# Optimization experiments

Hardware: AMD Instinct MI355X
Metric: run time of the kernel (lower is better)

Reference implementation:

```python
import jax, jax.numpy as jnp
import numpy as np

DIM = 256
DQK = DIM // 8
LN_SHAPE = (256, 4, 32, 32)


def setup_inputs() -> dict:
    key = jax.random.key(0)
    ks = jax.random.split(key, 12)
    B, C, Z, H, W = 4, 256, 4, 32, 32
    s = 0.02
    return {
        "x": jax.random.normal(ks[0], (B, C, Z, H, W), jnp.float32),
        "y": jax.random.normal(ks[1], (B, C, Z, H, W), jnp.float32),
        "Wq": jax.random.normal(ks[2], (DQK, C), jnp.float32) * s,
        "bq": jnp.zeros((DQK,), jnp.float32),
        "Wk": jax.random.normal(ks[3], (DQK, C), jnp.float32) * s,
        "bk": jnp.zeros((DQK,), jnp.float32),
        "Wv": jax.random.normal(ks[4], (C, C), jnp.float32) * s,
        "bv": jnp.zeros((C,), jnp.float32),
        "W1": jax.random.normal(ks[5], (C, C), jnp.float32) * s,
        "b1": jnp.zeros((C,), jnp.float32),
        "W2": jax.random.normal(ks[6], (C, C), jnp.float32) * s,
        "b2": jnp.zeros((C,), jnp.float32),
        "gamma": jnp.ones(LN_SHAPE, jnp.float32),
        "beta": jnp.zeros(LN_SHAPE, jnp.float32),
    }


def reference(x, y, Wq, bq, Wk, bk, Wv, bv, W1, b1, W2, b2, gamma, beta):
    B, C, Z, H, W = x.shape
    N = Z * H * W
    scale = (C // 8) ** (-0.5)

    def proj(t, Wm, bm):  # 1x1x1 conv3d == channel linear: [B,C,N] -> [B,out,N]
        return jnp.einsum('oc,bcn->bon', Wm, t.reshape(B, C, N)) + bm[None, :, None]

    def branch(a, b):
        q = proj(a, Wq, bq).transpose(0, 2, 1) * scale  # [B,N,dqk]
        k = proj(b, Wk, bk)                             # [B,dqk,N]
        v = proj(b, Wv, bv)                             # [B,C,N]
        attn = jax.nn.softmax(jnp.einsum('bnd,bdm->bnm', q, k), axis=-1)  # [B,N,N]
        out = jnp.einsum('bcm,bnm->bcn', v, attn).reshape(B, C, Z, H, W)
        h = out.transpose(0, 2, 3, 4, 1)  # [B,Z,H,W,C]
        h = jnp.maximum(jnp.einsum('bzhwc,oc->bzhwo', h, W1) + b1, 0.0)
        h = jnp.einsum('bzhwc,oc->bzhwo', h, W2) + b2
        h = h.transpose(0, 4, 1, 2, 3)  # [B,C,Z,H,W]
        mu = h.mean(axis=(1, 2, 3, 4), keepdims=True)
        var = h.var(axis=(1, 2, 3, 4), keepdims=True)
        return (h - mu) / jnp.sqrt(var + 1e-5) * gamma + beta

    return branch(x, y), branch(y, x)
```

## Files before the change

### kernel.cpp

```cpp
#include <hip/hip_runtime.h>

#define C_DIM 256
#define N_TOK 4096
#define DQK_  32
#define SCALE_Q 0.17677669529663687f

typedef unsigned short u16;
typedef __attribute__((ext_vector_type(8))) short bf16x8;
typedef __attribute__((ext_vector_type(16))) float f32x16;

__device__ __forceinline__ u16 f2b(float f) {
  unsigned u = __builtin_bit_cast(unsigned, f);
  unsigned r = (u + 0x7fffu + ((u >> 16) & 1u)) >> 16;
  return (u16)r;
}
__device__ __forceinline__ unsigned splitw(float v) {
  unsigned h = f2b(v);
  float hf = __builtin_bit_cast(float, h << 16);
  unsigned l = f2b(v - hf);
  return h | (l << 16);
}
__device__ __forceinline__ unsigned cvtpk(float lo, float hi) {
  unsigned r;
  asm("v_cvt_pk_bf16_f32 %0, %1, %2" : "=v"(r) : "v"(lo), "v"(hi));
  return r;
}

__global__ __launch_bounds__(256) void prep_kernel(
    const float* __restrict__ x, const float* __restrict__ y,
    u16* __restrict__ xhi, u16* __restrict__ yhi,
    const float* __restrict__ Wv, const float* __restrict__ W1, const float* __restrict__ W2,
    const float* __restrict__ Wq, const float* __restrict__ Wk,
    u16* __restrict__ Wvh, u16* __restrict__ Wvl,
    u16* __restrict__ W1h, u16* __restrict__ W1l,
    u16* __restrict__ W2h, u16* __restrict__ W2l,
    u16* __restrict__ Wqh, u16* __restrict__ Wql,
    u16* __restrict__ Wkh, u16* __restrict__ Wkl)
{
  __shared__ float tile[64][65];
  int bid = blockIdx.x;
  int t = threadIdx.x;
  if (bid < 2048) {
    int bx = bid & 63, by = (bid >> 6) & 3, z = bid >> 8;
    const float* src = (z < 4 ? x : y) + (size_t)(z & 3) * C_DIM * N_TOK;
    u16* dhi = (z < 4 ? xhi : yhi) + (size_t)(z & 3) * N_TOK * C_DIM;
    int m0 = bx * 64, c0 = by * 64;
    #pragma unroll
    for (int pp = 0; pp < 4; ++pp) {
      int c = pp*16 + (t >> 4), m = (t & 15)*4;
      float4 v = *(const float4*)(src + (size_t)(c0 + c)*N_TOK + m0 + m);
      tile[c][m] = v.x; tile[c][m+1] = v.y; tile[c][m+2] = v.z; tile[c][m+3] = v.w;
    }
    __syncthreads();
    int m = t >> 2, cg = (t & 3) * 16;
    unsigned hw[8];
    #pragma unroll
    for (int j2 = 0; j2 < 8; ++j2)
      hw[j2] = (unsigned)f2b(tile[cg + 2*j2][m]) | ((unsigned)f2b(tile[cg + 2*j2 + 1][m]) << 16);
    size_t base = (size_t)(m0 + m)*C_DIM + c0 + cg;
    *(uint4*)(dhi + base)     = make_uint4(hw[0], hw[1], hw[2], hw[3]);
    *(uint4*)(dhi + base + 8) = make_uint4(hw[4], hw[5], hw[6], hw[7]);
  } else {
    int wb = bid - 2048;
    int which, base;
    if (wb < 768) { which = wb >> 8; base = wb & 255; }
    else if (wb < 800) { which = 3; base = wb - 768; }
    else { which = 4; base = wb - 800; }
    const float* src = which == 0 ? Wv : which == 1 ? W1 : which == 2 ? W2 : which == 3 ? Wq : Wk;
    u16* dhi = which == 0 ? Wvh : which == 1 ? W1h : which == 2 ? W2h : which == 3 ? Wqh : Wkh;
    u16* dlo = which == 0 ? Wvl : which == 1 ? W1l : which == 2 ? W2l : which == 3 ? Wql : Wkl;
    int idx = base*256 + t;
    unsigned s = splitw(src[idx]);
    dhi[idx] = (u16)(s & 0xffffu);
    dlo[idx] = (u16)(s >> 16);
  }
}

__device__ __forceinline__ void gemm_v_body(
    char* lds, int bx, int by, int bb,
    const u16* __restrict__ Ahi0, const u16* __restrict__ Ahi1, size_t aStride,
    const u16* __restrict__ Bhi, const u16* __restrict__ Blo,
    const float* __restrict__ bias, u16* __restrict__ OutBase, size_t oStride)
{
  const u16* Ah = (bb < 4 ? Ahi0 : Ahi1) + (size_t)(bb & 3) * aStride;
  int l0 = bx * 128;
  int s0 = by * 128;
  u16* Ob = OutBase + (size_t)bb * oStride;

  char* ldsAh = lds;
  char* ldsBh = lds + 16384;
  char* ldsBl = lds + 32768;

  int t = threadIdx.x;
  int w = t >> 6, lane = t & 63, g = lane >> 5, l31 = lane & 31;
  int lw = (w & 1) * 64, sw = (w >> 1) * 64;
  int swz = (l31 & 7) << 4;

  f32x16 acc[2][2];
  #pragma unroll
  for (int i = 0; i < 2; ++i)
    #pragma unroll
    for (int j = 0; j < 2; ++j)
      #pragma unroll
      for (int r = 0; r < 16; ++r) acc[i][j][r] = 0.f;

  uint4 rAh[4], rBh[4], rBl[4];
  #pragma unroll
  for (int c = 0; c < 4; ++c) {
    int idx = c*256 + t, row = idx >> 3, slot = idx & 7;
    rAh[c] = *(const uint4*)(Ah  + (size_t)(l0 + row)*C_DIM + slot*8);
    rBh[c] = *(const uint4*)(Bhi + (size_t)(s0 + row)*C_DIM + slot*8);
    rBl[c] = *(const uint4*)(Blo + (size_t)(s0 + row)*C_DIM + slot*8);
  }
  for (int bk = 0; bk < 4; ++bk) {
    __syncthreads();
    #pragma unroll
    for (int c = 0; c < 4; ++c) {
      int idx = c*256 + t, row = idx >> 3, slot = idx & 7;
      int off = row*128 + ((slot*16) ^ ((row & 7) << 4));
      *(uint4*)(ldsAh + off) = rAh[c];
      *(uint4*)(ldsBh + off) = rBh[c];
      *(uint4*)(ldsBl + off) = rBl[c];
    }
    __syncthreads();
    if (bk < 3) {
      #pragma unroll
      for (int c = 0; c < 4; ++c) {
        int idx = c*256 + t, row = idx >> 3, slot = idx & 7;
        rAh[c] = *(const uint4*)(Ah  + (size_t)(l0 + row)*C_DIM + (bk+1)*64 + slot*8);
        rBh[c] = *(const uint4*)(Bhi + (size_t)(s0 + row)*C_DIM + (bk+1)*64 + slot*8);
        rBl[c] = *(const uint4*)(Blo + (size_t)(s0 + row)*C_DIM + (bk+1)*64 + slot*8);
      }
    }
    #pragma unroll
    for (int ks = 0; ks < 4; ++ks) {
      int ko = ks*32 + g*16;
      bf16x8 ah0 = *(const bf16x8*)(ldsAh + (lw + l31)*128      + (ko ^ swz));
      bf16x8 ah1 = *(const bf16x8*)(ldsAh + (lw + 32 + l31)*128 + (ko ^ swz));
      bf16x8 bh0 = *(const bf16x8*)(ldsBh + (sw + l31)*128      + (ko ^ swz));
      bf16x8 bh1 = *(const bf16x8*)(ldsBh + (sw + 32 + l31)*128 + (ko ^ swz));
      bf16x8 bl0 = *(const bf16x8*)(ldsBl + (sw + l31)*128      + (ko ^ swz));
      bf16x8 bl1 = *(const bf16x8*)(ldsBl + (sw + 32 + l31)*128 + (ko ^ swz));
      acc[0][0] = __builtin_amdgcn_mfma_f32_32x32x16_bf16(ah0, bh0, acc[0][0], 0,0,0);
      acc[0][1] = __builtin_amdgcn_mfma_f32_32x32x16_bf16(ah0, bh1, acc[0][1], 0,0,0);
      acc[1][0] = __builtin_amdgcn_mfma_f32_32x32x16_bf16(ah1, bh0, acc[1][0], 0,0,0);
      acc[1][1] = __builtin_amdgcn_mfma_f32_32x32x16_bf16(ah1, bh1, acc[1][1], 0,0,0);
      acc[0][0] = __builtin_amdgcn_mfma_f32_32x32x16_bf16(ah0, bl0, acc[0][0], 0,0,0);
      acc[0][1] = __builtin_amdgcn_mfma_f32_32x32x16_bf16(ah0, bl1, acc[0][1], 0,0,0);
      acc[1][0] = __builtin_amdgcn_mfma_f32_32x32x16_bf16(ah1, bl0, acc[1][0], 0,0,0);
      acc[1][1] = __builtin_amdgcn_mfma_f32_32x32x16_bf16(ah1, bl1, acc[1][1], 0,0,0);
    }
  }

  for (int h = 0; h < 2; ++h) {
    __syncthreads();
    if ((w >> 1) == h) {
      #pragma unroll
      for (int j = 0; j < 2; ++j) {
        int sl = j*32 + l31;
        float bv = bias[s0 + h*64 + sl];
        #pragma unroll
        for (int i = 0; i < 2; ++i)
          #pragma unroll
          for (int q = 0; q < 4; ++q) {
            int lbase = lw + i*32 + 8*q + 4*g;
            unsigned w0 = (unsigned)f2b(acc[i][j][q*4+0] + bv)
                        | ((unsigned)f2b(acc[i][j][q*4+1] + bv) << 16);
            unsigned w1 = (unsigned)f2b(acc[i][j][q*4+2] + bv)
                        | ((unsigned)f2b(acc[i][j][q*4+3] + bv) << 16);
            *(uint2*)(lds + sl*272 + lbase*2) = make_uint2(w0, w1);
          }
      }
    }
    __syncthreads();
    #pragma unroll
    for (int p = 0; p < 4; ++p) {
      int s = p*16 + (t >> 4), col = (t & 15)*8;
      uint4 v = *(const uint4*)(lds + s*272 + col*2);
      *(uint4*)(Ob + (size_t)(s0 + h*64 + s)*(size_t)N_TOK + l0 + col) = v;
    }
  }
}

__device__ __forceinline__ void proj_qk_body(
    char* lds, int bx, int which, int bb,
    const u16* __restrict__ xs_hi, const u16* __restrict__ ys_hi,
    const u16* __restrict__ Wqh, const u16* __restrict__ Wql,
    const u16* __restrict__ Wkh, const u16* __restrict__ Wkl,
    const float* __restrict__ bq, const float* __restrict__ bk,
    u16* __restrict__ Qout, u16* __restrict__ Kout)
{
  int branch = bb >> 2, batch = bb & 3;
  int n0 = bx * 256;
  const u16* Asrc = (which == 0 ? (branch ? ys_hi : xs_hi) : (branch ? xs_hi : ys_hi))
                    + (size_t)batch * N_TOK * C_DIM;
  const u16* Bh = which ? Wkh : Wqh;
  const u16* Bl = which ? Wkl : Wql;
  const float* bias = which ? bk : bq;
  float sc = which ? 1.0f : SCALE_Q;
  u16* out = (which ? Kout : Qout) + (size_t)bb * N_TOK * DQK_;

  char* ldsA  = lds;
  char* ldsBh = lds + 32768;
  char* ldsBl = lds + 40960;

  int t = threadIdx.x, w = t >> 6, lane = t & 63, g = lane >> 5, l31 = lane & 31;
  int swz = (l31 & 7) << 4;

  f32x16 acc[2];
  #pragma unroll
  for (int i = 0; i < 2; ++i)
    #pragma unroll
    for (int r = 0; r < 16; ++r) acc[i][r] = 0.f;

  uint4 rA[8]; uint4 rBh, rBl;
  #pragma unroll
  for (int c = 0; c < 8; ++c) {
    int idx = c*256 + t, row = idx >> 3, slot = idx & 7;
    rA[c] = *(const uint4*)(Asrc + (size_t)(n0 + row)*C_DIM + slot*8);
  }
  { int row = t >> 3, slot = t & 7;
    rBh = *(const uint4*)(Bh + (size_t)row*C_DIM + slot*8);
    rBl = *(const uint4*)(Bl + (size_t)row*C_DIM + slot*8); }

  for (int bk = 0; bk < 4; ++bk) {
    __syncthreads();
    #pragma unroll
    for (int c = 0; c < 8; ++c) {
      int idx = c*256 + t, row = idx >> 3, slot = idx & 7;
      *(uint4*)(ldsA + row*128 + ((slot*16) ^ ((row & 7) << 4))) = rA[c];
    }
    { int row = t >> 3, slot = t & 7;
      int off = row*128 + ((slot*16) ^ ((row & 7) << 4));
      *(uint4*)(ldsBh + off) = rBh;
      *(uint4*)(ldsBl + off) = rBl; }
    __syncthreads();
    if (bk < 3) {
      #pragma unroll
      for (int c = 0; c < 8; ++c) {
        int idx = c*256 + t, row = idx >> 3, slot = idx & 7;
        rA[c] = *(const uint4*)(Asrc + (size_t)(n0 + row)*C_DIM + (bk+1)*64 + slot*8);
      }
      { int row = t >> 3, slot = t & 7;
        rBh = *(const uint4*)(Bh + (size_t)row*C_DIM + (bk+1)*64 + slot*8);
        rBl = *(const uint4*)(Bl + (size_t)row*C_DIM + (bk+1)*64 + slot*8); }
    }
    #pragma unroll
    for (int ks = 0; ks < 4; ++ks) {
      int ko = ks*32 + g*16;
      bf16x8 a0 = *(const bf16x8*)(ldsA + (w*64 + l31)*128      + (ko ^ swz));
      bf16x8 a1 = *(const bf16x8*)(ldsA + (w*64 + 32 + l31)*128 + (ko ^ swz));
      bf16x8 bh = *(const bf16x8*)(ldsBh + l31*128 + (ko ^ swz));
      bf16x8 bl = *(const bf16x8*)(ldsBl + l31*128 + (ko ^ swz));
      acc[0] = __builtin_amdgcn_mfma_f32_32x32x16_bf16(a0, bh, acc[0], 0,0,0);
      acc[1] = __builtin_amdgcn_mfma_f32_32x32x16_bf16(a1, bh, acc[1], 0,0,0);
      acc[0] = __builtin_amdgcn_mfma_f32_32x32x16_bf16(a0, bl, acc[0], 0,0,0);
      acc[1] = __builtin_amdgcn_mfma_f32_32x32x16_bf16(a1, bl, acc[1], 0,0,0);
    }
  }
  float bv = bias[l31];
  #pragma unroll
  for (int sub = 0; sub < 2; ++sub)
    #pragma unroll
    for (int r = 0; r < 16; ++r) {
      int n = w*64 + sub*32 + (r&3) + 8*(r>>2) + 4*g;
      out[(size_t)(n0 + n)*DQK_ + l31] = f2b((acc[sub][r] + bv) * sc);
    }
}

__global__ __launch_bounds__(256) void pv_qk_kernel(
    const u16* __restrict__ xs_hi, const u16* __restrict__ ys_hi,
    const u16* __restrict__ Wvh, const u16* __restrict__ Wvl,
    const u16* __restrict__ Wqh, const u16* __restrict__ Wql,
    const u16* __restrict__ Wkh, const u16* __restrict__ Wkl,
    const float* __restrict__ bv, const float* __restrict__ bq, const float* __restrict__ bk,
    u16* __restrict__ Vt, u16* __restrict__ Qout, u16* __restrict__ Kout)
{
  __shared__ __align__(16) char lds[49152];
  int bid = blockIdx.x;
  const size_t AS = (size_t)N_TOK * C_DIM;
  if (bid < 512) {
    int bx = bid & 31, by = (bid >> 5) & 1, bb = bid >> 6;
    gemm_v_body(lds, bx, by, bb, ys_hi, xs_hi, AS, Wvh, Wvl, bv, Vt, AS);
  } else {
    int pb = bid - 512;
    int bx = pb & 15, which = (pb >> 4) & 1, bb = pb >> 5;
    proj_qk_body(lds, bx, which, bb, xs_hi, ys_hi, Wqh, Wql, Wkh, Wkl, bq, bk, Qout, Kout);
  }
}

__global__ __launch_bounds__(512) void attn_fused_kernel(
    const u16* __restrict__ Qg, const u16* __restrict__ Kg,
    const u16* __restrict__ Vtg, u16* __restrict__ Ohi)
{
  int id = blockIdx.x;
  int bb = id & 7;
  int n0 = (id >> 3) * 128;
  const u16* Qb = Qg + (size_t)bb * N_TOK * DQK_;
  const u16* Kb = Kg + (size_t)bb * N_TOK * DQK_;
  const u16* Vb = Vtg + (size_t)bb * C_DIM * N_TOK;
  u16* Ohb = Ohi + (size_t)bb * N_TOK * C_DIM;

  __shared__ __align__(16) u16 Kl[2][2][4*64*8];
  __shared__ __align__(16) u16 Vl[2][256*128];

  int t = threadIdx.x;
  int w = t >> 6;
  int grp = w >> 2;
  int wg = w & 3;
  int t4 = t & 255;
  int lane = t & 63, g = lane >> 5, l31 = lane & 31;

  bf16x8 qf0 = *(const bf16x8*)(Qb + (size_t)(n0 + wg*32 + l31)*DQK_ + g*8);
  bf16x8 qf1 = *(const bf16x8*)(Qb + (size_t)(n0 + wg*32 + l31)*DQK_ + 16 + g*8);

  f32x16 acc[8];
  #pragma unroll
  for (int ct = 0; ct < 8; ++ct)
    #pragma unroll
    for (int r = 0; r < 16; ++r) acc[ct][r] = 0.f;

  float L = 0.f;

  bf16x8 stK, stV[8];
  const u16* kSrc = Kb + (size_t)(grp*32*64 + (t4>>7)*32 + (t4&31))*DQK_
                       + ((t4>>6)&1)*16 + ((t4>>5)&1)*8;
  const int vCol0 = grp*32*64;
  stK = *(const bf16x8*)(kSrc);
  #pragma unroll
  for (int i = 0; i < 8; ++i) {
    int q = i*256 + t4;
    stV[i] = *(const bf16x8*)(Vb + (size_t)(q >> 3)*N_TOK + vCol0 + (q & 7)*8);
  }

  u16* VlG = Vl[grp];

  *(bf16x8*)(Kl[grp][0] + t4*8) = stK;
  #pragma unroll
  for (int i = 0; i < 8; ++i) {
    int q = i*256 + t4;
    int c = q >> 3, slot = q & 7;
    *(bf16x8*)((char*)VlG + c*256 + ((slot*16) ^ ((c & 15) << 4))) = stV[i];
  }
  __syncthreads();

  int h = 0;
  for (int mt = 0; mt < 32; ++mt) {
    const u16* KlG = Kl[grp][h];
    f32x16 z;
    #pragma unroll
    for (int r = 0; r < 16; ++r) z[r] = 0.f;
    bf16x8 ka = *(const bf16x8*)(KlG + (0*64 + lane)*8);
    bf16x8 kb = *(const bf16x8*)(KlG + (1*64 + lane)*8);
    bf16x8 kc = *(const bf16x8*)(KlG + (2*64 + lane)*8);
    bf16x8 kd = *(const bf16x8*)(KlG + (3*64 + lane)*8);
    f32x16 st0 = __builtin_amdgcn_mfma_f32_32x32x16_bf16(ka, qf0, z, 0,0,0);
    st0 = __builtin_amdgcn_mfma_f32_32x32x16_bf16(kb, qf1, st0, 0,0,0);
    f32x16 st1 = __builtin_amdgcn_mfma_f32_32x32x16_bf16(kc, qf0, z, 0,0,0);
    st1 = __builtin_amdgcn_mfma_f32_32x32x16_bf16(kd, qf1, st1, 0,0,0);

    if (mt + 1 < 32) {
      stK = *(const bf16x8*)(kSrc + (size_t)(mt+1)*64*DQK_);
      #pragma unroll
      for (int i = 0; i < 8; ++i) {
        int q = i*256 + t4;
        stV[i] = *(const bf16x8*)(Vb + (size_t)(q >> 3)*N_TOK + vCol0 + (mt+1)*64 + (q & 7)*8);
      }
    }

    float ps = 0.f;
    uint4 pav[4];
    #pragma unroll
    for (int msub = 0; msub < 2; ++msub) {
      f32x16 sv = msub ? st1 : st0;
      float p[16];
      #pragma unroll
      for (int r = 0; r < 16; ++r)
        p[r] = __expf(fminf(sv[r], 30.f));
      float q0 = (p[0]+p[1]) + (p[2]+p[3]);
      float q1 = (p[4]+p[5]) + (p[6]+p[7]);
      float q2 = (p[8]+p[9]) + (p[10]+p[11]);
      float q3 = (p[12]+p[13]) + (p[14]+p[15]);
      ps += (q0+q1) + (q2+q3);
      unsigned k0a = cvtpk(p[0],  p[1]),  k0b = cvtpk(p[2],  p[3]);
      unsigned k1a = cvtpk(p[4],  p[5]),  k1b = cvtpk(p[6],  p[7]);
      unsigned k2a = cvtpk(p[8],  p[9]),  k2b = cvtpk(p[10], p[11]);
      unsigned k3a = cvtpk(p[12], p[13]), k3b = cvtpk(p[14], p[15]);
      unsigned X1a = g ? k0a : k1a, X1b = g ? k0b : k1b;
      unsigned X2a = g ? k2a : k3a, X2b = g ? k2b : k3b;
      X1a = __shfl_xor(X1a, 32); X1b = __shfl_xor(X1b, 32);
      X2a = __shfl_xor(X2a, 32); X2b = __shfl_xor(X2b, 32);
      pav[msub*2]     = g ? make_uint4(X1a, X1b, k1a, k1b)
                          : make_uint4(k0a, k0b, X1a, X1b);
      pav[msub*2 + 1] = g ? make_uint4(X2a, X2b, k3a, k3b)
                          : make_uint4(k2a, k2b, X2a, X2b);
    }
    ps += __shfl_xor(ps, 32);
    L += ps;

    __builtin_amdgcn_s_setprio(1);
    #pragma unroll
    for (int ks = 0; ks < 4; ++ks) {
      bf16x8 pa = __builtin_bit_cast(bf16x8, pav[ks]);
      #pragma unroll
      for (int ct = 0; ct < 8; ++ct) {
        bf16x8 vv = *(const bf16x8*)((char*)VlG + (ct*32 + l31)*256
                     + ((h*128 + ks*32 + g*16) ^ ((l31 & 15) << 4)));
        acc[ct] = __builtin_amdgcn_mfma_f32_32x32x16_bf16(pa, vv, acc[ct], 0,0,0);
      }
    }
    __builtin_amdgcn_s_setprio(0);

    if (mt + 1 < 32) {
      *(bf16x8*)(Kl[grp][h ^ 1] + t4*8) = stK;
      #pragma unroll
      for (int i = 0; i < 8; ++i) {
        int q = i*256 + t4;
        int c = q >> 3, slot = q & 7;
        *(bf16x8*)((char*)VlG + c*256 + (((h ^ 1)*128 + slot*16) ^ ((c & 15) << 4))) = stV[i];
      }
    }
    __syncthreads();
    h ^= 1;
  }

  float* mb = (float*)Kl;
  mb[t] = L;
  __syncthreads();
  float Ln = L + mb[t ^ 256];

  float* vb = (float*)Vl;
  #pragma unroll
  for (int pass = 0; pass < 2; ++pass) {
    __syncthreads();
    if (grp == 1) {
      #pragma unroll
      for (int cc = 0; cc < 4; ++cc) {
        int ct = pass*4 + cc;
        #pragma unroll
        for (int r = 0; r < 16; ++r)
          vb[(cc*256 + t4)*16 + r] = acc[ct][r];
      }
    }
    __syncthreads();
    if (grp == 0) {
      #pragma unroll
      for (int cc = 0; cc < 4; ++cc) {
        int ct = pass*4 + cc;
        #pragma unroll
        for (int r = 0; r < 16; ++r)
          acc[ct][r] += vb[(cc*256 + t4)*16 + r];
      }
    }
  }

  if (grp == 0) {
    float lr = 1.0f / Ln;
    float lrr[16];
    #pragma unroll
    for (int r = 0; r < 16; ++r)
      lrr[r] = __shfl(lr, (r&3) + 8*(r>>2) + 4*g, 32);
    #pragma unroll
    for (int ct = 0; ct < 8; ++ct) {
      #pragma unroll
      for (int r = 0; r < 16; ++r) {
        int nr = (r&3) + 8*(r>>2) + 4*g;
        size_t off = (size_t)(n0 + wg*32 + nr)*C_DIM + ct*32 + l31;
        Ohb[off] = f2b(acc[ct][r] * lrr[r]);
      }
    }
  }
}

__global__ __launch_bounds__(512) void ffn_fused_kernel(
    const u16* __restrict__ Ohi, const u16* __restrict__ W1h, const u16* __restrict__ W1l,
    const u16* __restrict__ W2h, const u16* __restrict__ W2l,
    const float* __restrict__ b1, const float* __restrict__ b2,
    float* __restrict__ out, float* __restrict__ part)
{
  int bb = blockIdx.y;
  int l0 = blockIdx.x * 128;
  const u16* Ah = Ohi + (size_t)bb * N_TOK * C_DIM;
  float* Ob = out + (size_t)bb * (size_t)N_TOK * C_DIM;

  __shared__ __align__(16) char lds[147456];
  char* ldsH1 = lds;
  char* ldsA  = lds + 65536;
  char* ldsBh = lds + 81920;
  char* ldsBl = lds + 114688;

  int t = threadIdx.x;
  int w = t >> 6, lane = t & 63, g = lane >> 5, l31 = lane & 31;
  int lw = (w & 1) * 64, sw = (w >> 1) * 64;
  int swz = (l31 & 7) << 4;

  f32x16 acc[2][2];
  #pragma unroll
  for (int i = 0; i < 2; ++i)
    #pragma unroll
    for (int j = 0; j < 2; ++j)
      #pragma unroll
      for (int r = 0; r < 16; ++r) acc[i][j][r] = 0.f;

  uint4 rA[2], rBh[4], rBl[4];
  #pragma unroll
  for (int c = 0; c < 2; ++c) {
    int u = c*512 + t, row = u >> 3, slot = u & 7;
    rA[c] = *(const uint4*)(Ah + (size_t)(l0 + row)*C_DIM + slot*8);
  }
  #pragma unroll
  for (int c = 0; c < 4; ++c) {
    int u = c*512 + t, row = u >> 3, slot = u & 7;
    rBh[c] = *(const uint4*)(W1h + (size_t)row*C_DIM + slot*8);
    rBl[c] = *(const uint4*)(W1l + (size_t)row*C_DIM + slot*8);
  }
  for (int bk = 0; bk < 4; ++bk) {
    __syncthreads();
    #pragma unroll
    for (int c = 0; c < 2; ++c) {
      int u = c*512 + t, row = u >> 3, slot = u & 7;
      *(uint4*)(ldsA + row*128 + ((slot*16) ^ ((row & 7) << 4))) = rA[c];
    }
    #pragma unroll
    for (int c = 0; c < 4; ++c) {
      int u = c*512 + t, row = u >> 3, slot = u & 7;
      int off = row*128 + ((slot*16) ^ ((row & 7) << 4));
      *(uint4*)(ldsBh + off) = rBh[c];
      *(uint4*)(ldsBl + off) = rBl[c];
    }
    __syncthreads();
    if (bk < 3) {
      #pragma unroll
      for (int c = 0; c < 2; ++c) {
        int u = c*512 + t, row = u >> 3, slot = u & 7;
        rA[c] = *(const uint4*)(Ah + (size_t)(l0 + row)*C_DIM + (bk+1)*64 + slot*8);
      }
      #pragma unroll
      for (int c = 0; c < 4; ++c) {
        int u = c*512 + t, row = u >> 3, slot = u & 7;
        rBh[c] = *(const uint4*)(W1h + (size_t)row*C_DIM + (bk+1)*64 + slot*8);
        rBl[c] = *(const uint4*)(W1l + (size_t)row*C_DIM + (bk+1)*64 + slot*8);
      }
    }
    #pragma unroll
    for (int ks = 0; ks < 4; ++ks) {
      int ko = ks*32 + g*16;
      bf16x8 ah0 = *(const bf16x8*)(ldsA + (lw + l31)*128      + (ko ^ swz));
      bf16x8 ah1 = *(const bf16x8*)(ldsA + (lw + 32 + l31)*128 + (ko ^ swz));
      bf16x8 bh0 = *(const bf16x8*)(ldsBh + (sw + l31)*128      + (ko ^ swz));
      bf16x8 bh1 = *(const bf16x8*)(ldsBh + (sw + 32 + l31)*128 + (ko ^ swz));
      bf16x8 bl0 = *(const bf16x8*)(ldsBl + (sw + l31)*128      + (ko ^ swz));
      bf16x8 bl1 = *(const bf16x8*)(ldsBl + (sw + 32 + l31)*128 + (ko ^ swz));
      acc[0][0] = __builtin_amdgcn_mfma_f32_32x32x16_bf16(ah0, bh0, acc[0][0], 0,0,0);
      acc[0][1] = __builtin_amdgcn_mfma_f32_32x32x16_bf16(ah0, bh1, acc[0][1], 0,0,0);
      acc[1][0] = __builtin_amdgcn_mfma_f32_32x32x16_bf16(ah1, bh0, acc[1][0], 0,0,0);
      acc[1][1] = __builtin_amdgcn_mfma_f32_32x32x16_bf16(ah1, bh1, acc[1][1], 0,0,0);
      acc[0][0] = __builtin_amdgcn_mfma_f32_32x32x16_bf16(ah0, bl0, acc[0][0], 0,0,0);
      acc[0][1] = __builtin_amdgcn_mfma_f32_32x32x16_bf16(ah0, bl1, acc[0][1], 0,0,0);
      acc[1][0] = __builtin_amdgcn_mfma_f32_32x32x16_bf16(ah1, bl0, acc[1][0], 0,0,0);
      acc[1][1] = __builtin_amdgcn_mfma_f32_32x32x16_bf16(ah1, bl1, acc[1][1], 0,0,0);
    }
  }

  #pragma unroll
  for (int j = 0; j < 2; ++j) {
    int o = sw + j*32 + l31;
    float bv = b1[o];
    #pragma unroll
    for (int i = 0; i < 2; ++i)
      #pragma unroll
      for (int r = 0; r < 16; ++r) {
        int n = lw + i*32 + (r&3) + 8*(r>>2) + 4*g;
        *(u16*)(ldsH1 + n*512 + ((o*2) ^ ((n & 7) << 4))) = f2b(fmaxf(acc[i][j][r] + bv, 0.f));
      }
  }

  #pragma unroll
  for (int i = 0; i < 2; ++i)
    #pragma unroll
    for (int j = 0; j < 2; ++j)
      #pragma unroll
      for (int r = 0; r < 16; ++r) acc[i][j][r] = 0.f;

  #pragma unroll
  for (int c = 0; c < 4; ++c) {
    int u = c*512 + t, row = u >> 3, slot = u & 7;
    rBh[c] = *(const uint4*)(W2h + (size_t)row*C_DIM + slot*8);
    rBl[c] = *(const uint4*)(W2l + (size_t)row*C_DIM + slot*8);
  }
  for (int bk = 0; bk < 4; ++bk) {
    __syncthreads();
    #pragma unroll
    for (int c = 0; c < 4; ++c) {
      int u = c*512 + t, row = u >> 3, slot = u & 7;
      int off = row*128 + ((slot*16) ^ ((row & 7) << 4));
      *(uint4*)(ldsBh + off) = rBh[c];
      *(uint4*)(ldsBl + off) = rBl[c];
    }
    __syncthreads();
    if (bk < 3) {
      #pragma unroll
      for (int c = 0; c < 4; ++c) {
        int u = c*512 + t, row = u >> 3, slot = u & 7;
        rBh[c] = *(const uint4*)(W2h + (size_t)row*C_DIM + (bk+1)*64 + slot*8);
        rBl[c] = *(const uint4*)(W2l + (size_t)row*C_DIM + (bk+1)*64 + slot*8);
      }
    }
    #pragma unroll
    for (int ks = 0; ks < 4; ++ks) {
      int ko = ks*32 + g*16;
      int kb = bk*128 + ko;
      bf16x8 ah0 = *(const bf16x8*)(ldsH1 + (lw + l31)*512      + (kb ^ swz));
      bf16x8 ah1 = *(const bf16x8*)(ldsH1 + (lw + 32 + l31)*512 + (kb ^ swz));
      bf16x8 bh0 = *(const bf16x8*)(ldsBh + (sw + l31)*128      + (ko ^ swz));
      bf16x8 bh1 = *(const bf16x8*)(ldsBh + (sw + 32 + l31)*128 + (ko ^ swz));
      bf16x8 bl0 = *(const bf16x8*)(ldsBl + (sw + l31)*128      + (ko ^ swz));
      bf16x8 bl1 = *(const bf16x8*)(ldsBl + (sw + 32 + l31)*128 + (ko ^ swz));
      acc[0][0] = __builtin_amdgcn_mfma_f32_32x32x16_bf16(ah0, bh0, acc[0][0], 0,0,0);
      acc[0][1] = __builtin_amdgcn_mfma_f32_32x32x16_bf16(ah0, bh1, acc[0][1], 0,0,0);
      acc[1][0] = __builtin_amdgcn_mfma_f32_32x32x16_bf16(ah1, bh0, acc[1][0], 0,0,0);
      acc[1][1] = __builtin_amdgcn_mfma_f32_32x32x16_bf16(ah1, bh1, acc[1][1], 0,0,0);
      acc[0][0] = __builtin_amdgcn_mfma_f32_32x32x16_bf16(ah0, bl0, acc[0][0], 0,0,0);
      acc[0][1] = __builtin_amdgcn_mfma_f32_32x32x16_bf16(ah0, bl1, acc[0][1], 0,0,0);
      acc[1][0] = __builtin_amdgcn_mfma_f32_32x32x16_bf16(ah1, bl0, acc[1][0], 0,0,0);
      acc[1][1] = __builtin_amdgcn_mfma_f32_32x32x16_bf16(ah1, bl1, acc[1][1], 0,0,0);
    }
  }

  float s = 0.f, s2 = 0.f;
  #pragma unroll
  for (int j = 0; j < 2; ++j) {
    float bv = b2[sw + j*32 + l31];
    #pragma unroll
    for (int i = 0; i < 2; ++i)
      #pragma unroll
      for (int r = 0; r < 16; ++r) {
        acc[i][j][r] += bv;
        s += acc[i][j][r];
        s2 += acc[i][j][r]*acc[i][j][r];
      }
  }
  for (int off = 32; off; off >>= 1) {
    s  += __shfl_down(s, off, 64);
    s2 += __shfl_down(s2, off, 64);
  }
  __syncthreads();
  float* sc = (float*)(lds + 147456 - 64);
  if (lane == 0) { sc[w*2] = s; sc[w*2+1] = s2; }
  __syncthreads();
  if (t == 0) {
    int slot = bb*32 + blockIdx.x;
    float S = 0.f, S2 = 0.f;
    #pragma unroll
    for (int q = 0; q < 8; ++q) { S += sc[q*2]; S2 += sc[q*2+1]; }
    part[slot*2]     = S;
    part[slot*2 + 1] = S2;
  }

  for (int hh = 0; hh < 2; ++hh) {
    __syncthreads();
    if ((w >> 2) == hh) {
      #pragma unroll
      for (int j = 0; j < 2; ++j) {
        int sl = (sw - hh*128) + j*32 + l31;
        #pragma unroll
        for (int i = 0; i < 2; ++i)
          #pragma unroll
          for (int q = 0; q < 4; ++q) {
            int lbase = lw + i*32 + 8*q + 4*g;
            float4 vv;
            vv.x = acc[i][j][q*4+0];
            vv.y = acc[i][j][q*4+1];
            vv.z = acc[i][j][q*4+2];
            vv.w = acc[i][j][q*4+3];
            *(float4*)(lds + sl*528 + lbase*4) = vv;
          }
      }
    }
    __syncthreads();
    #pragma unroll
    for (int p = 0; p < 8; ++p) {
      int sl = p*16 + (t >> 5), col = (t & 31)*4;
      float4 v = *(const float4*)(lds + sl*528 + col*4);
      *(float4*)(Ob + (size_t)(hh*128 + sl)*(size_t)N_TOK + l0 + col) = v;
    }
  }
}

__global__ __launch_bounds__(256) void ln_apply_kernel(
    float* __restrict__ H, const float* __restrict__ gamma,
    const float* __restrict__ beta, const float* __restrict__ part)
{
  __shared__ float st[2];
  int base = blockIdx.x * 4096;
  int bb = base >> 20;
  int t = threadIdx.x;
  if (t < 64) {
    float s = 0.f, s2 = 0.f;
    if (t < 32) { s = part[(bb*32 + t)*2]; s2 = part[(bb*32 + t)*2 + 1]; }
    for (int off = 16; off; off >>= 1) {
      s  += __shfl_down(s, off, 64);
      s2 += __shfl_down(s2, off, 64);
    }
    if (t == 0) {
      float mean = s * (1.0f/1048576.0f);
      float var  = s2 * (1.0f/1048576.0f) - mean*mean;
      st[0] = mean;
      st[1] = rsqrtf(var + 1e-5f);
    }
  }
  __syncthreads();
  float mean = st[0], istd = st[1];
  #pragma unroll
  for (int k = 0; k < 4; ++k) {
    int e = base + (k*256 + t)*4;
    int rem = e & ((1 << 20) - 1);
    float4 h = *(float4*)(H + (size_t)e);
    float4 g = *(const float4*)(gamma + rem);
    float4 b = *(const float4*)(beta + rem);
    h.x = (h.x - mean)*istd*g.x + b.x;
    h.y = (h.y - mean)*istd*g.y + b.y;
    h.z = (h.z - mean)*istd*g.z + b.z;
    h.w = (h.w - mean)*istd*g.w + b.w;
    *(float4*)(H + (size_t)e) = h;
  }
}

extern "C" void kernel_launch(void* const* d_in, const int* in_sizes, int n_in,
                              void* d_out, int out_size, void* d_ws, size_t ws_size,
                              hipStream_t stream) {
  (void)in_sizes; (void)n_in; (void)out_size; (void)ws_size;
  const float* x  = (const float*)d_in[0];
  const float* y  = (const float*)d_in[1];
  const float* Wq = (const float*)d_in[2];
  const float* bq = (const float*)d_in[3];
  const float* Wk = (const float*)d_in[4];
  const float* bk = (const float*)d_in[5];
  const float* Wv = (const float*)d_in[6];
  const float* bv = (const float*)d_in[7];
  const float* W1 = (const float*)d_in[8];
  const float* b1 = (const float*)d_in[9];
  const float* W2 = (const float*)d_in[10];
  const float* b2 = (const float*)d_in[11];
  const float* gamma = (const float*)d_in[12];
  const float* beta  = (const float*)d_in[13];
  float* out = (float*)d_out;

  char* ws = (char*)d_ws;
  u16* xs_hi = (u16*)(ws);
  u16* ys_hi = (u16*)(ws + (8ull<<20));
  u16* Q     = (u16*)(ws + (16ull<<20));
  u16* Kp    = (u16*)(ws + (18ull<<20));
  u16* Vt    = (u16*)(ws + (20ull<<20));
  u16* Ohi   = (u16*)(ws);
  u16* Wvh   = (u16*)(ws + (52ull<<20));
  u16* Wvl   = Wvh + 65536;
  u16* W1h   = Wvh + 2*65536;
  u16* W1l   = Wvh + 3*65536;
  u16* W2h   = Wvh + 4*65536;
  u16* W2l   = Wvh + 5*65536;
  u16* Wqh   = Wvh + 6*65536;
  u16* Wql   = Wqh + 8192;
  u16* Wkh   = Wqh + 2*8192;
  u16* Wkl   = Wqh + 3*8192;
  float* part  = (float*)(ws + (53ull<<20));

  prep_kernel <<<2880, 256, 0, stream>>>(
      x, y, xs_hi, ys_hi, Wv, W1, W2, Wq, Wk,
      Wvh, Wvl, W1h, W1l, W2h, W2l, Wqh, Wql, Wkh, Wkl);
  pv_qk_kernel<<<768, 256, 0, stream>>>(
      xs_hi, ys_hi, Wvh, Wvl, Wqh, Wql, Wkh, Wkl, bv, bq, bk, Vt, Q, Kp);
  attn_fused_kernel<<<256, 512, 0, stream>>>(Q, Kp, Vt, Ohi);
  ffn_fused_kernel <<<dim3(32,8), 512, 0, stream>>>(
      Ohi, W1h, W1l, W2h, W2l, b1, b2, out, part);
  ln_apply_kernel  <<<2048, 256, 0, stream>>>(out, gamma, beta, part);
}
```

Baseline: 244.9 us.

## Fuse attention output with FFN in one kernel via LDS handoff

Merges the attention kernel and the two-layer FFN kernel into one kernel. Each block keeps its normalized attention output tile in swizzled LDS as the A operand for the first FFN GEMM. This removes the bf16 Ohi round trip through global memory and one kernel launch. In exchange the attention kernel now reserves 144KB of LDS, which can limit occupancy, and the output write-out is split into four passes because of LDS reuse.

```diff
diff --git a/kernel.cpp b/kernel.cpp
--- a/kernel.cpp
+++ b/kernel.cpp
@@ -289,20 +289,24 @@
   }
 }
 
-__global__ __launch_bounds__(512) void attn_fused_kernel(
+__global__ __launch_bounds__(512) void attn_ffn_kernel(
     const u16* __restrict__ Qg, const u16* __restrict__ Kg,
-    const u16* __restrict__ Vtg, u16* __restrict__ Ohi)
+    const u16* __restrict__ Vtg,
+    const u16* __restrict__ W1h, const u16* __restrict__ W1l,
+    const u16* __restrict__ W2h, const u16* __restrict__ W2l,
+    const float* __restrict__ b1, const float* __restrict__ b2,
+    float* __restrict__ out, float* __restrict__ part)
 {
+  __shared__ __align__(16) char lds[147456];
   int id = blockIdx.x;
   int bb = id & 7;
   int n0 = (id >> 3) * 128;
   const u16* Qb = Qg + (size_t)bb * N_TOK * DQK_;
   const u16* Kb = Kg + (size_t)bb * N_TOK * DQK_;
   const u16* Vb = Vtg + (size_t)bb * C_DIM * N_TOK;
-  u16* Ohb = Ohi + (size_t)bb * N_TOK * C_DIM;
-
-  __shared__ __align__(16) u16 Kl[2][2][4*64*8];
-  __shared__ __align__(16) u16 Vl[2][256*128];
+
+  u16* Kl = (u16*)lds;
+  u16* Vl = (u16*)(lds + 16384);
 
   int t = threadIdx.x;
   int w = t >> 6;
@@ -310,6 +314,7 @@
   int wg = w & 3;
   int t4 = t & 255;
   int lane = t & 63, g = lane >> 5, l31 = lane & 31;
+  int swz = (l31 & 7) << 4;
 
   bf16x8 qf0 = *(const bf16x8*)(Qb + (size_t)(n0 + wg*32 + l31)*DQK_ + g*8);
   bf16x8 qf1 = *(const bf16x8*)(Qb + (size_t)(n0 + wg*32 + l31)*DQK_ + 16 + g*8);
@@ -333,9 +338,9 @@
     stV[i] = *(const bf16x8*)(Vb + (size_t)(q >> 3)*N_TOK + vCol0 + (q & 7)*8);
   }
 
-  u16* VlG = Vl[grp];
-
-  *(bf16x8*)(Kl[grp][0] + t4*8) = stK;
+  u16* VlG = Vl + grp*32768;
+
+  *(bf16x8*)(Kl + grp*4096 + t4*8) = stK;
   #pragma unroll
   for (int i = 0; i < 8; ++i) {
     int q = i*256 + t4;
@@ -346,7 +351,7 @@
 
   int h = 0;
   for (int mt = 0; mt < 32; ++mt) {
-    const u16* KlG = Kl[grp][h];
+    const u16* KlG = Kl + grp*4096 + h*2048;
     f32x16 z;
     #pragma unroll
     for (int r = 0; r < 16; ++r) z[r] = 0.f;
@@ -412,7 +417,7 @@
     __builtin_amdgcn_s_setprio(0);
 
     if (mt + 1 < 32) {
-      *(bf16x8*)(Kl[grp][h ^ 1] + t4*8) = stK;
+      *(bf16x8*)(Kl + grp*4096 + (h^1)*2048 + t4*8) = stK;
       #pragma unroll
       for (int i = 0; i < 8; ++i) {
         int q = i*256 + t4;
@@ -453,7 +458,9 @@
       }
     }
   }
-
+  __syncthreads();
+
+  char* ldsO = lds + 16384;
   if (grp == 0) {
     float lr = 1.0f / Ln;
     float lrr[16];
@@ -464,50 +471,30 @@
     for (int ct = 0; ct < 8; ++ct) {
       #pragma unroll
       for (int r = 0; r < 16; ++r) {
-        int nr = (r&3) + 8*(r>>2) + 4*g;
-        size_t off = (size_t)(n0 + wg*32 + nr)*C_DIM + ct*32 + l31;
-        Ohb[off] = f2b(acc[ct][r] * lrr[r]);
-      }
-    }
-  }
-}
-
-__global__ __launch_bounds__(512) void ffn_fused_kernel(
-    const u16* __restrict__ Ohi, const u16* __restrict__ W1h, const u16* __restrict__ W1l,
-    const u16* __restrict__ W2h, const u16* __restrict__ W2l,
-    const float* __restrict__ b1, const float* __restrict__ b2,
-    float* __restrict__ out, float* __restrict__ part)
-{
-  int bb = blockIdx.y;
-  int l0 = blockIdx.x * 128;
-  const u16* Ah = Ohi + (size_t)bb * N_TOK * C_DIM;
-  float* Ob = out + (size_t)bb * (size_t)N_TOK * C_DIM;
-
-  __shared__ __align__(16) char lds[147456];
-  char* ldsH1 = lds;
-  char* ldsA  = lds + 65536;
-  char* ldsBh = lds + 81920;
-  char* ldsBl = lds + 114688;
-
-  int t = threadIdx.x;
-  int w = t >> 6, lane = t & 63, g = lane >> 5, l31 = lane & 31;
+        int n = wg*32 + (r&3) + 8*(r>>2) + 4*g;
+        int c = ct*32 + l31;
+        *(u16*)(ldsO + n*512 + ((c*2) ^ ((n & 7) << 4))) = f2b(acc[ct][r] * lrr[r]);
+      }
+    }
+  }
+  __syncthreads();
+
   int lw = (w & 1) * 64, sw = (w >> 1) * 64;
-  int swz = (l31 & 7) << 4;
-
-  f32x16 acc[2][2];
+  char* ldsH1  = lds + 81920;
+  char* ldsBh1 = lds + 81920;
+  char* ldsBl1 = lds + 114688;
+  char* ldsBh2 = lds + 16384;
+  char* ldsBl2 = lds + 49152;
+
+  f32x16 fa[2][2];
   #pragma unroll
   for (int i = 0; i < 2; ++i)
     #pragma unroll
     for (int j = 0; j < 2; ++j)
       #pragma unroll
-      for (int r = 0; r < 16; ++r) acc[i][j][r] = 0.f;
-
-  uint4 rA[2], rBh[4], rBl[4];
-  #pragma unroll
-  for (int c = 0; c < 2; ++c) {
-    int u = c*512 + t, row = u >> 3, slot = u & 7;
-    rA[c] = *(const uint4*)(Ah + (size_t)(l0 + row)*C_DIM + slot*8);
-  }
+      for (int r = 0; r < 16; ++r) fa[i][j][r] = 0.f;
+
+  uint4 rBh[4], rBl[4];
   #pragma unroll
   for (int c = 0; c < 4; ++c) {
     int u = c*512 + t, row = u >> 3, slot = u & 7;
@@ -517,24 +504,14 @@
   for (int bk = 0; bk < 4; ++bk) {
     __syncthreads();
     #pragma unroll
-    for (int c = 0; c < 2; ++c) {
-      int u = c*512 + t, row = u >> 3, slot = u & 7;
-      *(uint4*)(ldsA + row*128 + ((slot*16) ^ ((row & 7) << 4))) = rA[c];
-    }
-    #pragma unroll
     for (int c = 0; c < 4; ++c) {
       int u = c*512 + t, row = u >> 3, slot = u & 7;
       int off = row*128 + ((slot*16) ^ ((row & 7) << 4));
-      *(uint4*)(ldsBh + off) = rBh[c];
-      *(uint4*)(ldsBl + off) = rBl[c];
+      *(uint4*)(ldsBh1 + off) = rBh[c];
+      *(uint4*)(ldsBl1 + off) = rBl[c];
     }
     __syncthreads();
     if (bk < 3) {
-      #pragma unroll
-      for (int c = 0; c < 2; ++c) {
-        int u = c*512 + t, row = u >> 3, slot = u & 7;
-        rA[c] = *(const uint4*)(Ah + (size_t)(l0 + row)*C_DIM + (bk+1)*64 + slot*8);
-      }
       #pragma unroll
       for (int c = 0; c < 4; ++c) {
         int u = c*512 + t, row = u >> 3, slot = u & 7;
@@ -545,33 +522,35 @@
     #pragma unroll
     for (int ks = 0; ks < 4; ++ks) {
       int ko = ks*32 + g*16;
-      bf16x8 ah0 = *(const bf16x8*)(ldsA + (lw + l31)*128      + (ko ^ swz));
-      bf16x8 ah1 = *(const bf16x8*)(ldsA + (lw + 32 + l31)*128 + (ko ^ swz));
-      bf16x8 bh0 = *(const bf16x8*)(ldsBh + (sw + l31)*128      + (ko ^ swz));
-      bf16x8 bh1 = *(const bf16x8*)(ldsBh + (sw + 32 + l31)*128 + (ko ^ swz));
-      bf16x8 bl0 = *(const bf16x8*)(ldsBl + (sw + l31)*128      + (ko ^ swz));
-      bf16x8 bl1 = *(const bf16x8*)(ldsBl + (sw + 32 + l31)*128 + (ko ^ swz));
-      acc[0][0] = __builtin_amdgcn_mfma_f32_32x32x16_bf16(ah0, bh0, acc[0][0], 0,0,0);
-      acc[0][1] = __builtin_amdgcn_mfma_f32_32x32x16_bf16(ah0, bh1, acc[0][1], 0,0,0);
-      acc[1][0] = __builtin_amdgcn_mfma_f32_32x32x16_bf16(ah1, bh0, acc[1][0], 0,0,0);
-      acc[1][1] = __builtin_amdgcn_mfma_f32_32x32x16_bf16(ah1, bh1, acc[1][1], 0,0,0);
-      acc[0][0] = __builtin_amdgcn_mfma_f32_32x32x16_bf16(ah0, bl0, acc[0][0], 0,0,0);
-      acc[0][1] = __builtin_amdgcn_mfma_f32_32x32x16_bf16(ah0, bl1, acc[0][1], 0,0,0);
-      acc[1][0] = __builtin_amdgcn_mfma_f32_32x32x16_bf16(ah1, bl0, acc[1][0], 0,0,0);
-      acc[1][1] = __builtin_amdgcn_mfma_f32_32x32x16_bf16(ah1, bl1, acc[1][1], 0,0,0);
-    }
-  }
+      int kb = bk*128 + ko;
+      bf16x8 ah0 = *(const bf16x8*)(ldsO + (lw + l31)*512      + (kb ^ swz));
+      bf16x8 ah1 = *(const bf16x8*)(ldsO + (lw + 32 + l31)*512 + (kb ^ swz));
+      bf16x8 bh0 = *(const bf16x8*)(ldsBh1 + (sw + l31)*128      + (ko ^ swz));
+      bf16x8 bh1 = *(const bf16x8*)(ldsBh1 + (sw + 32 + l31)*128 + (ko ^ swz));
+      bf16x8 bl0 = *(const bf16x8*)(ldsBl1 + (sw + l31)*128      + (ko ^ swz));
+      bf16x8 bl1 = *(const bf16x8*)(ldsBl1 + (sw + 32 + l31)*128 + (ko ^ swz));
+      fa[0][0] = __builtin_amdgcn_mfma_f32_32x32x16_bf16(ah0, bh0, fa[0][0], 0,0,0);
+      fa[0][1] = __builtin_amdgcn_mfma_f32_32x32x16_bf16(ah0, bh1, fa[0][1], 0,0,0);
+      fa[1][0] = __builtin_amdgcn_mfma_f32_32x32x16_bf16(ah1, bh0, fa[1][0], 0,0,0);
+      fa[1][1] = __builtin_amdgcn_mfma_f32_32x32x16_bf16(ah1, bh1, fa[1][1], 0,0,0);
+      fa[0][0] = __builtin_amdgcn_mfma_f32_32x32x16_bf16(ah0, bl0, fa[0][0], 0,0,0);
+      fa[0][1] = __builtin_amdgcn_mfma_f32_32x32x16_bf16(ah0, bl1, fa[0][1], 0,0,0);
+      fa[1][0] = __builtin_amdgcn_mfma_f32_32x32x16_bf16(ah1, bl0, fa[1][0], 0,0,0);
+      fa[1][1] = __builtin_amdgcn_mfma_f32_32x32x16_bf16(ah1, bl1, fa[1][1], 0,0,0);
+    }
+  }
+  __syncthreads();
 
   #pragma unroll
   for (int j = 0; j < 2; ++j) {
     int o = sw + j*32 + l31;
-    float bv = b1[o];
+    float bvv = b1[o];
     #pragma unroll
     for (int i = 0; i < 2; ++i)
       #pragma unroll
       for (int r = 0; r < 16; ++r) {
         int n = lw + i*32 + (r&3) + 8*(r>>2) + 4*g;
-        *(u16*)(ldsH1 + n*512 + ((o*2) ^ ((n & 7) << 4))) = f2b(fmaxf(acc[i][j][r] + bv, 0.f));
+        *(u16*)(ldsH1 + n*512 + ((o*2) ^ ((n & 7) << 4))) = f2b(fmaxf(fa[i][j][r] + bvv, 0.f));
       }
   }
 
@@ -580,7 +559,7 @@
     #pragma unroll
     for (int j = 0; j < 2; ++j)
       #pragma unroll
-      for (int r = 0; r < 16; ++r) acc[i][j][r] = 0.f;
+      for (int r = 0; r < 16; ++r) fa[i][j][r] = 0.f;
 
   #pragma unroll
   for (int c = 0; c < 4; ++c) {
@@ -594,8 +573,8 @@
     for (int c = 0; c < 4; ++c) {
       int u = c*512 + t, row = u >> 3, slot = u & 7;
       int off = row*128 + ((slot*16) ^ ((row & 7) << 4));
-      *(uint4*)(ldsBh + off) = rBh[c];
-      *(uint4*)(ldsBl + off) = rBl[c];
+      *(uint4*)(ldsBh2 + off) = rBh[c];
+      *(uint4*)(ldsBl2 + off) = rBl[c];
     }
     __syncthreads();
     if (bk < 3) {
@@ -612,32 +591,32 @@
       int kb = bk*128 + ko;
       bf16x8 ah0 = *(const bf16x8*)(ldsH1 + (lw + l31)*512      + (kb ^ swz));
       bf16x8 ah1 = *(const bf16x8*)(ldsH1 + (lw + 32 + l31)*512 + (kb ^ swz));
-      bf16x8 bh0 = *(const bf16x8*)(ldsBh + (sw + l31)*128      + (ko ^ swz));
-      bf16x8 bh1 = *(const bf16x8*)(ldsBh + (sw + 32 + l31)*128 + (ko ^ swz));
-      bf16x8 bl0 = *(const bf16x8*)(ldsBl + (sw + l31)*128      + (ko ^ swz));
-      bf16x8 bl1 = *(const bf16x8*)(ldsBl + (sw + 32 + l31)*128 + (ko ^ swz));
-      acc[0][0] = __builtin_amdgcn_mfma_f32_32x32x16_bf16(ah0, bh0, acc[0][0], 0,0,0);
-      acc[0][1] = __builtin_amdgcn_mfma_f32_32x32x16_bf16(ah0, bh1, acc[0][1], 0,0,0);
-      acc[1][0] = __builtin_amdgcn_mfma_f32_32x32x16_bf16(ah1, bh0, acc[1][0], 0,0,0);
-      acc[1][1] = __builtin_amdgcn_mfma_f32_32x32x16_bf16(ah1, bh1, acc[1][1], 0,0,0);
-      acc[0][0] = __builtin_amdgcn_mfma_f32_32x32x16_bf16(ah0, bl0, acc[0][0], 0,0,0);
-      acc[0][1] = __builtin_amdgcn_mfma_f32_32x32x16_bf16(ah0, bl1, acc[0][1], 0,0,0);
-      acc[1][0] = __builtin_amdgcn_mfma_f32_32x32x16_bf16(ah1, bl0, acc[1][0], 0,0,0);
-      acc[1][1] = __builtin_amdgcn_mfma_f32_32x32x16_bf16(ah1, bl1, acc[1][1], 0,0,0);
+      bf16x8 bh0 = *(const bf16x8*)(ldsBh2 + (sw + l31)*128      + (ko ^ swz));
+      bf16x8 bh1 = *(const bf16x8*)(ldsBh2 + (sw + 32 + l31)*128 + (ko ^ swz));
+      bf16x8 bl0 = *(const bf16x8*)(ldsBl2 + (sw + l31)*128      + (ko ^ swz));
+      bf16x8 bl1 = *(const bf16x8*)(ldsBl2 + (sw + 32 + l31)*128 + (ko ^ swz));
+      fa[0][0] = __builtin_amdgcn_mfma_f32_32x32x16_bf16(ah0, bh0, fa[0][0], 0,0,0);
+      fa[0][1] = __builtin_amdgcn_mfma_f32_32x32x16_bf16(ah0, bh1, fa[0][1], 0,0,0);
+      fa[1][0] = __builtin_amdgcn_mfma_f32_32x32x16_bf16(ah1, bh0, fa[1][0], 0,0,0);
+      fa[1][1] = __builtin_amdgcn_mfma_f32_32x32x16_bf16(ah1, bh1, fa[1][1], 0,0,0);
+      fa[0][0] = __builtin_amdgcn_mfma_f32_32x32x16_bf16(ah0, bl0, fa[0][0], 0,0,0);
+      fa[0][1] = __builtin_amdgcn_mfma_f32_32x32x16_bf16(ah0, bl1, fa[0][1], 0,0,0);
+      fa[1][0] = __builtin_amdgcn_mfma_f32_32x32x16_bf16(ah1, bl0, fa[1][0], 0,0,0);
+      fa[1][1] = __builtin_amdgcn_mfma_f32_32x32x16_bf16(ah1, bl1, fa[1][1], 0,0,0);
     }
   }
 
   float s = 0.f, s2 = 0.f;
   #pragma unroll
   for (int j = 0; j < 2; ++j) {
-    float bv = b2[sw + j*32 + l31];
+    float bvv = b2[sw + j*32 + l31];
     #pragma unroll
     for (int i = 0; i < 2; ++i)
       #pragma unroll
       for (int r = 0; r < 16; ++r) {
-        acc[i][j][r] += bv;
-        s += acc[i][j][r];
-        s2 += acc[i][j][r]*acc[i][j][r];
+        fa[i][j][r] += bvv;
+        s += fa[i][j][r];
+        s2 += fa[i][j][r]*fa[i][j][r];
       }
   }
   for (int off = 32; off; off >>= 1) {
@@ -645,11 +624,11 @@
     s2 += __shfl_down(s2, off, 64);
   }
   __syncthreads();
-  float* sc = (float*)(lds + 147456 - 64);
+  float* sc = (float*)lds;
   if (lane == 0) { sc[w*2] = s; sc[w*2+1] = s2; }
   __syncthreads();
   if (t == 0) {
-    int slot = bb*32 + blockIdx.x;
+    int slot = bb*32 + (id >> 3);
     float S = 0.f, S2 = 0.f;
     #pragma unroll
     for (int q = 0; q < 8; ++q) { S += sc[q*2]; S2 += sc[q*2+1]; }
@@ -657,32 +636,35 @@
     part[slot*2 + 1] = S2;
   }
 
-  for (int hh = 0; hh < 2; ++hh) {
-    __syncthreads();
-    if ((w >> 2) == hh) {
+  float* Ob = out + (size_t)bb * (size_t)N_TOK * C_DIM;
+  int l0 = n0;
+  for (int qp = 0; qp < 4; ++qp) {
+    __syncthreads();
+    if ((w >> 1) == qp) {
       #pragma unroll
       for (int j = 0; j < 2; ++j) {
-        int sl = (sw - hh*128) + j*32 + l31;
+        int sl = j*32 + l31;
         #pragma unroll
         for (int i = 0; i < 2; ++i)
           #pragma unroll
           for (int q = 0; q < 4; ++q) {
             int lbase = lw + i*32 + 8*q + 4*g;
             float4 vv;
-            vv.x = acc[i][j][q*4+0];
-            vv.y = acc[i][j][q*4+1];
-            vv.z = acc[i][j][q*4+2];
-            vv.w = acc[i][j][q*4+3];
-            *(float4*)(lds + sl*528 + lbase*4) = vv;
+            vv.x = fa[i][j][q*4+0];
+            vv.y = fa[i][j][q*4+1];
+            vv.z = fa[i][j][q*4+2];
+            vv.w = fa[i][j][q*4+3];
+            *(float4*)(ldsO + sl*528 + lbase*4) = vv;
           }
       }
     }
     __syncthreads();
     #pragma unroll
-    for (int p = 0; p < 8; ++p) {
-      int sl = p*16 + (t >> 5), col = (t & 31)*4;
-      float4 v = *(const float4*)(lds + sl*528 + col*4);
-      *(float4*)(Ob + (size_t)(hh*128 + sl)*(size_t)N_TOK + l0 + col) = v;
+    for (int p2 = 0; p2 < 4; ++p2) {
+      int idx = p2*512 + t;
+      int sl = idx >> 5, col = (idx & 31)*4;
+      float4 v = *(const float4*)(ldsO + sl*528 + col*4);
+      *(float4*)(Ob + (size_t)(qp*64 + sl)*(size_t)N_TOK + l0 + col) = v;
     }
   }
 }
@@ -752,7 +734,6 @@
   u16* Q     = (u16*)(ws + (16ull<<20));
   u16* Kp    = (u16*)(ws + (18ull<<20));
   u16* Vt    = (u16*)(ws + (20ull<<20));
-  u16* Ohi   = (u16*)(ws);
   u16* Wvh   = (u16*)(ws + (52ull<<20));
   u16* Wvl   = Wvh + 65536;
   u16* W1h   = Wvh + 2*65536;
@@ -770,8 +751,7 @@
       Wvh, Wvl, W1h, W1l, W2h, W2l, Wqh, Wql, Wkh, Wkl);
   pv_qk_kernel<<<768, 256, 0, stream>>>(
       xs_hi, ys_hi, Wvh, Wvl, Wqh, Wql, Wkh, Wkl, bv, bq, bk, Vt, Q, Kp);
-  attn_fused_kernel<<<256, 512, 0, stream>>>(Q, Kp, Vt, Ohi);
-  ffn_fused_kernel <<<dim3(32,8), 512, 0, stream>>>(
-      Ohi, W1h, W1l, W2h, W2l, b1, b2, out, part);
-  ln_apply_kernel  <<<2048, 256, 0, stream>>>(out, gamma, beta, part);
-}
+  attn_ffn_kernel<<<256, 512, 0, stream>>>(
+      Q, Kp, Vt, W1h, W1l, W2h, W2l, b1, b2, out, part);
+  ln_apply_kernel <<<2048, 256, 0, stream>>>(out, gamma, beta, part);
+}
```

After: 218.3 us, median of 2. 1.12x faster.
